# Kernel optimization log

Hardware: AMD Instinct MI355X
Metric: run time of the kernel (lower is better)

The kernel has to match this reference:

```python
import jax, jax.numpy as jnp
import numpy as np

# GemNet-OC hyperparameters (match init_kwargs)
CUTOFF = 6.0
NR = 128     # num_radial
NS = 7       # num_spherical
NB = 2       # num_blocks
DA = 256     # emb_size_atom
DE = 512     # emb_size_edge
DT = 64      # emb_size_trip
DC = 16      # emb_size_cbf/rbf
NRES_M = 2   # edge residual layers per block (before+after skip)
NRES_H = 2   # atom residual layers per block (num_atom)
N_ELEM = 119
INV_SQRT2 = 0.7071067811865476
_GAMMA = 0.5 / (CUTOFF / NR) ** 2  # gaussian rbf width


def _radial_basis(d):
    """Gaussian RBF with polynomial envelope (exponent 5). d: [E] -> [E, NR]."""
    u = d / CUTOFF
    p = 5.0
    env = 1.0 - (p + 1) * (p + 2) / 2 * u**5 + p * (p + 2) * u**6 - p * (p + 1) / 2 * u**7
    env = jnp.where(u < 1.0, env, 0.0)
    mu = jnp.linspace(0.0, CUTOFF, NR, dtype=d.dtype)
    return env[:, None] * jnp.exp(-_GAMMA * (d[:, None] - mu) ** 2)


def setup_inputs() -> dict:
    key = jax.random.key(0)
    ks = jax.random.split(key, 32)
    N, E, T = 8000, 100000, 500000

    atomic_numbers = jax.random.randint(ks[0], (N,), 0, N_ELEM)
    edge_index = jax.random.randint(ks[1], (2, E), 0, N)
    distances = jax.random.uniform(ks[2], (E,), jnp.float32, 0.5, CUTOFF)
    id3_ba = jax.random.randint(ks[3], (T,), 0, E)
    id3_ca = jax.random.randint(ks[4], (T,), 0, E)
    cos_angles = jax.random.uniform(ks[5], (T,), jnp.float32, -0.99, 0.99)

    def w(k, shape, fan_in):
        return jax.random.normal(k, shape, jnp.float32) / np.sqrt(fan_in)

    params = dict(
        atom_table=w(ks[6], (N_ELEM, DA), 1.0),
        W_edge=w(ks[7], (2 * DA + NR, DE), 2 * DA + NR), b_edge=jnp.zeros((DE,), jnp.float32),
        W_rbf3=w(ks[8], (NR, DC), NR),
        W_sph=w(ks[9], (NS, DC), NS),
        W_cbf_up=w(ks[10], (DC, DT), DC),
        W_rbf_h=w(ks[11], (NR, DE), NR),
        W_ba=w(ks[12], (NB, DE, DE), DE), b_ba=jnp.zeros((NB, DE), jnp.float32),
        W_down=w(ks[13], (NB, DE, DT), DE),
        W_trip_up=w(ks[14], (NB, DT, DE), DT),
        W_res_m=w(ks[15], (NB, NRES_M, 2, DE, DE), DE), b_res_m=jnp.zeros((NB, NRES_M, 2, DE), jnp.float32),
        W_e2a=w(ks[16], (NB, DE, DA), DE),
        W_res_h=w(ks[17], (NB, NRES_H, 2, DA, DA), DA), b_res_h=jnp.zeros((NB, NRES_H, 2, DA), jnp.float32),
        W_out=w(ks[18], (DA, 1), DA),
    )
    return dict(atomic_numbers=atomic_numbers, edge_index=edge_index, distances=distances,
                id3_ba=id3_ba, id3_ca=id3_ca, cos_angles=cos_angles, **params)


def reference(atomic_numbers, edge_index, distances, id3_ba, id3_ca, cos_angles,
              atom_table, W_edge, b_edge, W_rbf3, W_sph, W_cbf_up, W_rbf_h,
              W_ba, b_ba, W_down, W_trip_up, W_res_m, b_res_m, W_e2a,
              W_res_h, b_res_h, W_out):
    N = atomic_numbers.shape[0]
    E = distances.shape[0]
    silu = jax.nn.silu

    # --- shared basis functions ---
    rbf = _radial_basis(distances)                               # [E, NR]
    theta = jnp.arccos(jnp.clip(cos_angles, -1.0, 1.0))
    sph = jnp.cos(theta[:, None] * jnp.arange(NS, dtype=theta.dtype))  # [T, NS]
    # circular basis embedding: radial part (gathered per triplet) x angular part
    cbf_emb = (rbf @ W_rbf3)[id3_ba] * (sph @ W_sph)             # [T, DC]
    cbf_up = cbf_emb @ W_cbf_up                                  # [T, DT]
    rbf_h = rbf @ W_rbf_h                                        # [E, DE]

    # --- embeddings ---
    src, tgt = edge_index[0], edge_index[1]
    h = atom_table[atomic_numbers]                               # [N, DA]
    m = silu(jnp.concatenate([h[src], h[tgt], rbf], axis=-1) @ W_edge + b_edge)  # [E, DE]

    def residual(x, Wr, br):  # Wr: [2, D, D], br: [2, D]
        y = silu(x @ Wr[0] + br[0])
        y = silu(y @ Wr[1] + br[1])
        return (x + y) * INV_SQRT2

    # --- interaction blocks ---
    for b in range(NB):
        # triplet message passing (edge -> triplet gather, triplet -> edge scatter)
        x_ba = silu(m @ W_ba[b] + b_ba[b]) @ W_down[b]           # [E, DT]
        x3 = jax.ops.segment_sum(x_ba[id3_ba] * cbf_up, id3_ca, num_segments=E)  # [E, DT]
        m = (m + x3 @ W_trip_up[b]) * INV_SQRT2
        for r in range(NRES_M):
            m = residual(m, W_res_m[b, r], b_res_m[b, r])
        # atom update: rbf-scaled edge messages scattered onto target atoms
        h_msg = jax.ops.segment_sum((m * rbf_h) @ W_e2a[b], tgt, num_segments=N)  # [N, DA]
        h = h + h_msg
        for r in range(NRES_H):
            h = residual(h, W_res_h[b, r], b_res_h[b, r])

    # --- extensive energy output ---
    energy = jnp.sum(h @ W_out)
    return energy
```

## Files before the change

### kernel.cpp

```cpp
#include <hip/hip_runtime.h>
#include <hip/hip_bf16.h>
#include <math.h>

#define CUTOFF 6.0f
#define NRAD 128
#define NSPH 7
#define DA 256
#define DE 512
#define DT 64
#define DCB 16
#define INV_SQRT2 0.7071067811865476f
#define RBF_GAMMA 227.55555555555554f

typedef __hip_bfloat16 bf16;
typedef __bf16 bf16v;
typedef bf16v bf16x8 __attribute__((ext_vector_type(8)));
typedef float f32x4 __attribute__((ext_vector_type(4)));

static inline int cdiv(int a, int b) { return (a + b - 1) / b; }

__device__ __forceinline__ float silu_f(float v) {
    return v / (1.0f + __expf(-v));
}

__device__ __forceinline__ float to_f(float v) { return v; }
__device__ __forceinline__ float to_f(bf16 v) { return __bfloat162float(v); }

template<typename T> __device__ __forceinline__ T from_f(float v);
template<> __device__ __forceinline__ float from_f<float>(float v) { return v; }
template<> __device__ __forceinline__ bf16 from_f<bf16>(float v) { return __float2bfloat16(v); }

#if defined(__has_builtin)
#if __has_builtin(__builtin_amdgcn_global_load_lds)
#define HAS_GLD 1
#endif
#endif

#ifdef HAS_GLD
__device__ __forceinline__ void gld16(const bf16* g, bf16* l) {
    __builtin_amdgcn_global_load_lds(
        (const __attribute__((address_space(1))) void*)g,
        (__attribute__((address_space(3))) void*)l, 16, 0, 0);
}
#endif

template<typename TC, typename TD, int GMODE, bool PRE_ADD, bool HAS_BIAS,
         bool ACT, bool POST_ADD, bool POST_MUL>
__global__ __launch_bounds__(512, 8)
void gemm_mfma(const bf16* __restrict__ A, const bf16* __restrict__ A3,
               const bf16* __restrict__ Bt,
               TC* __restrict__ C, const TC* __restrict__ Cin,
               const TD* __restrict__ Dop, const float* __restrict__ bias,
               const int* __restrict__ idx1, const int* __restrict__ idx2,
               int M, int N, int K, int lda, int ldb, float scale)
{
    __shared__ bf16 As[128 * 32];
    __shared__ bf16 Bs[128 * 32];
    const int tid = threadIdx.x;

    const int nwg = gridDim.x * gridDim.y;
    const int bid = blockIdx.y * gridDim.x + blockIdx.x;
    const int q = nwg >> 3, r = nwg & 7;
    const int xcd = bid & 7, jj = bid >> 3;
    const int wg = (xcd < r) ? (xcd * (q + 1) + jj) : (r + xcd * q + jj);
    const int bn = (wg % gridDim.x) * 128;
    const int bm = (wg / gridDim.x) * 128;

    const int w   = tid >> 6;
    const int l   = tid & 63;
    const int l16 = l & 15;
    const int lr4 = (l >> 4) * 4;
    const int wr  = (w >> 2) * 64;
    const int wc  = (w & 3) * 32;
    const int koff = (((l >> 4) ^ ((l16 >> 1) & 3)) << 3);

    f32x4 acc[4][2];
#pragma unroll
    for (int i = 0; i < 4; ++i)
#pragma unroll
        for (int j = 0; j < 2; ++j) acc[i][j] = (f32x4){0.f, 0.f, 0.f, 0.f};

    const int csw = (((l & 3) ^ ((l >> 3) & 3)) << 3);
    const int rA = w * 16 + (l >> 2);

    int ar = bm + rA; if (ar >= M) ar = M - 1;
    const bf16* pAa = A + (long)((GMODE >= 2) ? idx1[ar] : ar) * lda + csw;
    const bf16* pAb = (GMODE >= 2) ? (A + (long)idx2[ar] * lda + csw) : pAa;
    const bf16* pAc = (GMODE == 3) ? (A3 + (long)ar * NRAD + csw) : pAa;

    int bc = bn + rA; if (bc >= N) bc = N - 1;
    const bf16* pB = Bt + (long)bc * ldb + csw;

    bf16* ldsA = As + (w * 16) * 32;
    bf16* ldsB = Bs + (w * 16) * 32;

    for (int k0 = 0; k0 < K; k0 += 32) {
        const bf16* a0;
        if (GMODE == 0) {
            a0 = pAa + k0;
        } else if (GMODE == 2) {
            a0 = (k0 >= DA) ? (pAb + (k0 - DA)) : (pAa + k0);
        } else {
            if (k0 >= 2 * DA)  a0 = pAc + (k0 - 2 * DA);
            else if (k0 >= DA) a0 = pAb + (k0 - DA);
            else               a0 = pAa + k0;
        }
#ifdef HAS_GLD
        gld16(a0, ldsA);
        gld16(pB + k0, ldsB);
#else
        *(uint4*)(ldsA + (l >> 2) * 32 + (l & 3) * 8) = *(const uint4*)a0;
        *(uint4*)(ldsB + (l >> 2) * 32 + (l & 3) * 8) = *(const uint4*)(pB + k0);
#endif
        __syncthreads();

        bf16x8 bfr[2];
#pragma unroll
        for (int fn = 0; fn < 2; ++fn)
            bfr[fn] = *(const bf16x8*)&Bs[(wc + fn * 16 + l16) * 32 + koff];
#pragma unroll
        for (int fm = 0; fm < 4; ++fm) {
            bf16x8 af = *(const bf16x8*)&As[(wr + fm * 16 + l16) * 32 + koff];
            acc[fm][0] = __builtin_amdgcn_mfma_f32_16x16x32_bf16(af, bfr[0], acc[fm][0], 0, 0, 0);
            acc[fm][1] = __builtin_amdgcn_mfma_f32_16x16x32_bf16(af, bfr[1], acc[fm][1], 0, 0, 0);
        }
        __syncthreads();
    }

#pragma unroll
    for (int fm = 0; fm < 4; ++fm) {
#pragma unroll
        for (int fn = 0; fn < 2; ++fn) {
            const int col = bn + wc + fn * 16 + l16;
            if (col < N) {
#pragma unroll
                for (int r4 = 0; r4 < 4; ++r4) {
                    const int row = bm + wr + fm * 16 + lr4 + r4;
                    if (row < M) {
                        float v = acc[fm][fn][r4];
                        if (PRE_ADD)  v += to_f(Cin[(long)row * N + col]);
                        if (HAS_BIAS) v += bias[col];
                        if (ACT)      v = silu_f(v);
                        if (POST_ADD) v += to_f(Dop[(long)row * N + col]);
                        if (POST_MUL) v *= to_f(Dop[(long)row * N + col]);
                        C[(long)row * N + col] = from_f<TC>(v * scale);
                    }
                }
            }
        }
    }
}

__global__ void f2b_kernel(const float* __restrict__ in, bf16* __restrict__ out, long n)
{
    long i = ((long)blockIdx.x * 256 + threadIdx.x) * 4;
    const long stride = (long)gridDim.x * 256 * 4;
    for (; i < n; i += stride) {
        float4 v = *(const float4*)(in + i);
        bf16 o[4] = {__float2bfloat16(v.x), __float2bfloat16(v.y),
                     __float2bfloat16(v.z), __float2bfloat16(v.w)};
        *(ushort4*)(out + i) = *(const ushort4*)o;
    }
}

__global__ __launch_bounds__(256)
void t2bT_kernel(const float* __restrict__ in, bf16* __restrict__ out, int K, int Nc)
{
    __shared__ float tile[32][33];
    const long bofs = (long)blockIdx.z * K * Nc;
    const int k0 = blockIdx.y * 32;
    const int n0 = blockIdx.x * 32;
    const int tx = threadIdx.x & 31;
    const int ty = threadIdx.x >> 5;
#pragma unroll
    for (int i = 0; i < 4; ++i) {
        int k = k0 + ty + 8 * i;
        tile[ty + 8 * i][tx] = (k < K && n0 + tx < Nc) ? in[bofs + (long)k * Nc + n0 + tx] : 0.f;
    }
    __syncthreads();
#pragma unroll
    for (int i = 0; i < 4; ++i) {
        int n = n0 + ty + 8 * i;
        if (n < Nc && k0 + tx < K)
            out[bofs + (long)n * K + k0 + tx] = from_f<bf16>(tile[tx][ty + 8 * i]);
    }
}

__global__ __launch_bounds__(128)
void basis_kernel(const float* __restrict__ dist,
                  const float* __restrict__ W_rbf3,
                  bf16* __restrict__ rbf, bf16* __restrict__ rbf3, int E)
{
    __shared__ float s_rbf[NRAD];
    const int e = blockIdx.x;
    if (e >= E) return;
    const int k = threadIdx.x;
    const float d = dist[e];
    const float u = d * (1.0f / CUTOFF);
    float u2 = u * u, u4 = u2 * u2, u5 = u4 * u, u6 = u5 * u, u7 = u6 * u;
    float env = 1.0f - 21.0f * u5 + 35.0f * u6 - 15.0f * u7;
    if (u >= 1.0f) env = 0.0f;
    const float mu = CUTOFF * (float)k / (float)(NRAD - 1);
    const float t = d - mu;
    const float v = env * __expf(-RBF_GAMMA * t * t);
    s_rbf[k] = v;
    rbf[(long)e * NRAD + k] = __float2bfloat16(v);
    __syncthreads();

    if (k < DCB) {
        float acc = 0.f;
        for (int kk = 0; kk < NRAD; ++kk) acc += s_rbf[kk] * W_rbf3[kk * DCB + k];
        rbf3[(long)e * DCB + k] = __float2bfloat16(acc);
    }
}

__global__ void h_init_kernel(const int* __restrict__ an,
                              const float* __restrict__ table,
                              float* __restrict__ h, int N)
{
    int i = blockIdx.x * 256 + threadIdx.x;
    if (i < N * DA) {
        int a = i >> 8;
        int c = i & 255;
        h[i] = table[(long)an[a] * DA + c];
    }
}

__global__ void zeroi_kernel(int* __restrict__ p, int n)
{
    int i = blockIdx.x * 256 + threadIdx.x;
    if (i < n) p[i] = 0;
}
__global__ void copyi_kernel(const int* __restrict__ a, int* __restrict__ b, int n)
{
    int i = blockIdx.x * 256 + threadIdx.x;
    if (i < n) b[i] = a[i];
}
__global__ void count_kernel(const int* __restrict__ idx, int* __restrict__ cnt, int n)
{
    int i = blockIdx.x * 256 + threadIdx.x;
    if (i < n) atomicAdd(&cnt[idx[i]], 1);
}
__global__ __launch_bounds__(256)
void seg_p1(const int* __restrict__ cnt, int* __restrict__ bsum, int n)
{
    __shared__ int s[256];
    int i = blockIdx.x * 256 + threadIdx.x;
    s[threadIdx.x] = (i < n) ? cnt[i] : 0;
    __syncthreads();
    for (int o = 128; o > 0; o >>= 1) {
        if (threadIdx.x < o) s[threadIdx.x] += s[threadIdx.x + o];
        __syncthreads();
    }
    if (threadIdx.x == 0) bsum[blockIdx.x] = s[0];
}
__global__ __launch_bounds__(1024)
void seg_p2(int* __restrict__ bsum, int* __restrict__ off, int nb, int n)
{
    __shared__ int s[1024];
    int v = (threadIdx.x < nb) ? bsum[threadIdx.x] : 0;
    s[threadIdx.x] = v;
    __syncthreads();
    for (int o = 1; o < 1024; o <<= 1) {
        int t = (threadIdx.x >= o) ? s[threadIdx.x - o] : 0;
        __syncthreads();
        s[threadIdx.x] += t;
        __syncthreads();
    }
    if (threadIdx.x < nb) bsum[threadIdx.x] = s[threadIdx.x] - v;
    if (threadIdx.x == nb - 1) off[n] = s[threadIdx.x];
}
__global__ __launch_bounds__(256)
void seg_p3(const int* __restrict__ cnt, const int* __restrict__ bsum,
            int* __restrict__ off, int n)
{
    __shared__ int s[256];
    int i = blockIdx.x * 256 + threadIdx.x;
    int v = (i < n) ? cnt[i] : 0;
    s[threadIdx.x] = v;
    __syncthreads();
    for (int o = 1; o < 256; o <<= 1) {
        int t = (threadIdx.x >= o) ? s[threadIdx.x - o] : 0;
        __syncthreads();
        s[threadIdx.x] += t;
        __syncthreads();
    }
    if (i < n) off[i] = bsum[blockIdx.x] + s[threadIdx.x] - v;
}
__global__ void fill_kernel(const int* __restrict__ idx, int* __restrict__ cur,
                            int* __restrict__ list, int n)
{
    int i = blockIdx.x * 256 + threadIdx.x;
    if (i < n) {
        int p = atomicAdd(&cur[idx[i]], 1);
        list[p] = i;
    }
}

__global__ __launch_bounds__(256)
void emb16_kernel(const float* __restrict__ cosang,
                  const int* __restrict__ id3_ba,
                  const bf16* __restrict__ rbf3,
                  const float* __restrict__ W_sph,
                  bf16* __restrict__ emb, int T)
{
    __shared__ float s_W[NSPH * DCB];
    const int tid = threadIdx.x;
    if (tid < NSPH * DCB) s_W[tid] = W_sph[tid];
    __syncthreads();
    const long idx = (long)blockIdx.x * 256 + tid;
    if (idx >= (long)T * DCB) return;
    const int t = (int)(idx >> 4);
    const int cc = (int)(idx & 15);
    float c = cosang[t];
    c = fminf(1.0f, fmaxf(-1.0f, c));
    float s0 = 1.0f, s1 = c;
    float a = s_W[0 * DCB + cc] + c * s_W[1 * DCB + cc];
#pragma unroll
    for (int s = 2; s < NSPH; ++s) {
        float s2 = 2.0f * c * s1 - s0;
        a += s2 * s_W[s * DCB + cc];
        s0 = s1; s1 = s2;
    }
    emb[idx] = __float2bfloat16(a * to_f(rbf3[(long)id3_ba[t] * DCB + cc]));
}

__global__ __launch_bounds__(256)
void x3_gather_kernel(const int* __restrict__ ca_off, const int* __restrict__ ca_list,
                      const int* __restrict__ id3_ba,
                      const bf16* __restrict__ emb, const bf16* __restrict__ xba,
                      const float* __restrict__ W_up,
                      bf16* __restrict__ x3, int E)
{
    __shared__ float s_Wup[DCB * DT];
    const int tid = threadIdx.x;
    for (int i = tid; i < DCB * DT; i += 256) s_Wup[i] = W_up[i];
    __syncthreads();
    const int e = blockIdx.x * 4 + (tid >> 6);
    const int d = tid & 63;
    if (e >= E) return;
    const int j0 = ca_off[e], j1 = ca_off[e + 1];
    float acc = 0.f;
    for (int j = j0; j < j1; ++j) {
        const int t = ca_list[j];
        const int ba = id3_ba[t];
        const ushort* ep = (const ushort*)(emb + (long)t * DCB);
        float dotv = 0.f;
#pragma unroll
        for (int cc = 0; cc < DCB; ++cc)
            dotv += __uint_as_float((unsigned)ep[cc] << 16) * s_Wup[cc * DT + d];
        acc += dotv * to_f(xba[(long)ba * DT + d]);
    }
    x3[(long)e * DT + d] = from_f<bf16>(acc);
}

__global__ __launch_bounds__(256)
void atom_segsum_kernel(const int* __restrict__ tgt_off, const int* __restrict__ tgt_list,
                        const bf16* __restrict__ g, bf16* __restrict__ s_out, int N)
{
    const int a = blockIdx.x;
    if (a >= N) return;
    const int c = threadIdx.x;
    float acc0 = 0.f, acc1 = 0.f;
    const int j0 = tgt_off[a], j1 = tgt_off[a + 1];
    for (int j = j0; j < j1; ++j) {
        const bf16* row = g + (long)tgt_list[j] * DE;
        acc0 += to_f(row[c]);
        acc1 += to_f(row[c + 256]);
    }
    s_out[(long)a * DE + c]       = from_f<bf16>(acc0);
    s_out[(long)a * DE + c + 256] = from_f<bf16>(acc1);
}

__global__ __launch_bounds__(256)
void reduce1_kernel(const float* __restrict__ h, const float* __restrict__ Wout,
                    float* __restrict__ partials, int N)
{
    __shared__ float s[256];
    const int a0 = blockIdx.x * 32;
    const int col = threadIdx.x;
    float acc = 0.f;
    for (int a = 0; a < 32; ++a) {
        int row = a0 + a;
        if (row < N) acc += h[(long)row * DA + col];
    }
    acc *= Wout[col];
    s[col] = acc;
    __syncthreads();
    for (int off = 128; off > 0; off >>= 1) {
        if (col < off) s[col] += s[col + off];
        __syncthreads();
    }
    if (col == 0) partials[blockIdx.x] = s[0];
}

__global__ __launch_bounds__(256)
void reduce2_kernel(const float* __restrict__ partials, float* __restrict__ out, int nb)
{
    __shared__ float s[256];
    float acc = 0.f;
    for (int i = threadIdx.x; i < nb; i += 256) acc += partials[i];
    s[threadIdx.x] = acc;
    __syncthreads();
    for (int off = 128; off > 0; off >>= 1) {
        if (threadIdx.x < off) s[threadIdx.x] += s[threadIdx.x + off];
        __syncthreads();
    }
    if (threadIdx.x == 0) out[0] = s[0];
}

__global__ void diag_kernel(float* out, float v) { out[0] = v; }

extern "C" void kernel_launch(void* const* d_in, const int* in_sizes, int n_in,
                              void* d_out, int out_size, void* d_ws, size_t ws_size,
                              hipStream_t stream)
{
    const int*   atomic_numbers = (const int*)d_in[0];
    const int*   edge_index     = (const int*)d_in[1];
    const float* distances      = (const float*)d_in[2];
    const int*   id3_ba         = (const int*)d_in[3];
    const int*   id3_ca         = (const int*)d_in[4];
    const float* cos_angles     = (const float*)d_in[5];
    const float* atom_table     = (const float*)d_in[6];
    const float* W_edge         = (const float*)d_in[7];
    const float* b_edge         = (const float*)d_in[8];
    const float* W_rbf3         = (const float*)d_in[9];
    const float* W_sph          = (const float*)d_in[10];
    const float* W_cbf_up       = (const float*)d_in[11];
    const float* W_rbf_h        = (const float*)d_in[12];
    const float* W_ba           = (const float*)d_in[13];
    const float* b_ba           = (const float*)d_in[14];
    const float* W_down         = (const float*)d_in[15];
    const float* W_trip_up      = (const float*)d_in[16];
    const float* W_res_m        = (const float*)d_in[17];
    const float* b_res_m        = (const float*)d_in[18];
    const float* W_e2a          = (const float*)d_in[19];
    const float* W_res_h        = (const float*)d_in[20];
    const float* b_res_h        = (const float*)d_in[21];
    const float* W_out          = (const float*)d_in[22];

    const int N = in_sizes[0];
    const int E = in_sizes[2];
    const int T = in_sizes[3];
    const int* src = edge_index;
    const int* tgt = edge_index + E;

    char* base = (char*)d_ws;
    size_t off = 0;
    auto alloc = [&](size_t bytes) -> void* {
        void* r = base + off;
        off += (bytes + 255) & ~(size_t)255;
        return r;
    };
    bf16*  m     = (bf16*)alloc((size_t)E * DE * 2);
    bf16*  t1    = (bf16*)alloc((size_t)E * DE * 2);
    bf16*  rbf   = (bf16*)alloc((size_t)E * NRAD * 2);
    bf16*  rbf3  = (bf16*)alloc((size_t)E * DCB * 2);
    bf16*  xba   = (bf16*)alloc((size_t)E * DT * 2);
    float* h     = (float*)alloc((size_t)N * DA * 4);
    float* partials = (float*)alloc(4096 * 4);
    bf16* wedgeT = (bf16*)alloc((size_t)DE * (2 * DA + NRAD) * 2);
    bf16* wbaT   = (bf16*)alloc((size_t)2 * DE * DE * 2);
    bf16* wdownT = (bf16*)alloc((size_t)2 * DT * DE * 2);
    bf16* wtripT = (bf16*)alloc((size_t)2 * DE * DT * 2);
    bf16* wresmT = (bf16*)alloc((size_t)8 * DE * DE * 2);
    bf16* we2aT  = (bf16*)alloc((size_t)2 * DA * DE * 2);
    bf16* wrbfhT = (bf16*)alloc((size_t)DE * NRAD * 2);
    bf16* h_bf   = (bf16*)alloc((size_t)N * DA * 2);
    int* tgt_off  = (int*)alloc((size_t)(N + 1) * 4);
    int* tgt_list = (int*)alloc((size_t)E * 4);
    int* ca_off   = (int*)alloc((size_t)(E + 1) * 4);
    int* ca_list  = (int*)alloc((size_t)T * 4);
    bf16*  x3b    = t1;
    bf16*  emb16  = (bf16*)((char*)t1 + 20000000);
    bf16*  wreshT = (bf16*)((char*)t1 + 40000000);
    int*   cur_a  = (int*)t1;
    int*   cur_b  = (int*)((char*)t1 + 4000000);
    int*   bsum   = (int*)((char*)t1 + 8000000);
    bf16*  s_bf   = xba;
    bf16*  tmph_b = xba;

    if (off > ws_size) {
        diag_kernel<<<1, 1, 0, stream>>>((float*)d_out, (float)(ws_size >> 20));
        return;
    }

    const dim3 blk(256);
    const dim3 blk5(512);

    { dim3 g(DE / 32, (2 * DA + NRAD) / 32, 1);
      t2bT_kernel<<<g, blk, 0, stream>>>(W_edge, wedgeT, 2 * DA + NRAD, DE); }
    { dim3 g(DE / 32, DE / 32, 2);
      t2bT_kernel<<<g, blk, 0, stream>>>(W_ba, wbaT, DE, DE); }
    { dim3 g(DT / 32, DE / 32, 2);
      t2bT_kernel<<<g, blk, 0, stream>>>(W_down, wdownT, DE, DT); }
    { dim3 g(DE / 32, DT / 32, 2);
      t2bT_kernel<<<g, blk, 0, stream>>>(W_trip_up, wtripT, DT, DE); }
    { dim3 g(DE / 32, DE / 32, 8);
      t2bT_kernel<<<g, blk, 0, stream>>>(W_res_m, wresmT, DE, DE); }
    { dim3 g(DA / 32, DE / 32, 2);
      t2bT_kernel<<<g, blk, 0, stream>>>(W_e2a, we2aT, DE, DA); }
    { dim3 g(DE / 32, NRAD / 32, 1);
      t2bT_kernel<<<g, blk, 0, stream>>>(W_rbf_h, wrbfhT, NRAD, DE); }

    {
        zeroi_kernel<<<cdiv(N, 256), blk, 0, stream>>>(cur_a, N);
        count_kernel<<<cdiv(E, 256), blk, 0, stream>>>(tgt, cur_a, E);
        seg_p1<<<cdiv(N, 256), blk, 0, stream>>>(cur_a, bsum, N);
        seg_p2<<<1, 1024, 0, stream>>>(bsum, tgt_off, cdiv(N, 256), N);
        seg_p3<<<cdiv(N, 256), blk, 0, stream>>>(cur_a, bsum, tgt_off, N);
        copyi_kernel<<<cdiv(N, 256), blk, 0, stream>>>(tgt_off, cur_a, N);
        fill_kernel<<<cdiv(E, 256), blk, 0, stream>>>(tgt, cur_a, tgt_list, E);
        zeroi_kernel<<<cdiv(E, 256), blk, 0, stream>>>(cur_b, E);
        count_kernel<<<cdiv(T, 256), blk, 0, stream>>>(id3_ca, cur_b, T);
        seg_p1<<<cdiv(E, 256), blk, 0, stream>>>(cur_b, bsum, E);
        seg_p2<<<1, 1024, 0, stream>>>(bsum, ca_off, cdiv(E, 256), E);
        seg_p3<<<cdiv(E, 256), blk, 0, stream>>>(cur_b, bsum, ca_off, E);
        copyi_kernel<<<cdiv(E, 256), blk, 0, stream>>>(ca_off, cur_b, E);
        fill_kernel<<<cdiv(T, 256), blk, 0, stream>>>(id3_ca, cur_b, ca_list, T);
    }

    basis_kernel<<<E, 128, 0, stream>>>(distances, W_rbf3, rbf, rbf3, E);
    h_init_kernel<<<cdiv(N * DA, 256), blk, 0, stream>>>(atomic_numbers, atom_table, h, N);
    f2b_kernel<<<256, blk, 0, stream>>>(h, h_bf, (long)N * DA);

    {
        dim3 g(cdiv(DE, 128), cdiv(E, 128));
        gemm_mfma<bf16, bf16, 3, false, true, true, false, false>
            <<<g, blk5, 0, stream>>>(h_bf, rbf, wedgeT, m, nullptr, nullptr, b_edge,
                                     src, tgt, E, DE, 2 * DA + NRAD, DA, 2 * DA + NRAD, 1.0f);
    }

    for (int b = 0; b < 2; ++b) {
        const bf16* WbaT = wbaT + (long)b * DE * DE;
        const float* bba = b_ba + (long)b * DE;
        const bf16* WdnT = wdownT + (long)b * DT * DE;
        const bf16* WtuT = wtripT + (long)b * DE * DT;
        const bf16* We2aT = we2aT + (long)b * DA * DE;

        {
            dim3 g(cdiv(DE, 128), cdiv(E, 128));
            gemm_mfma<bf16, bf16, 0, false, true, true, false, false>
                <<<g, blk5, 0, stream>>>(m, nullptr, WbaT, t1, nullptr, (const bf16*)nullptr,
                                         bba, nullptr, nullptr, E, DE, DE, DE, DE, 1.0f);
        }
        {
            dim3 g(cdiv(DT, 128), cdiv(E, 128));
            gemm_mfma<bf16, bf16, 0, false, false, false, false, false>
                <<<g, blk5, 0, stream>>>(t1, nullptr, WdnT, xba, nullptr, (const bf16*)nullptr,
                                         nullptr, nullptr, nullptr, E, DT, DE, DE, DE, 1.0f);
        }
        emb16_kernel<<<cdiv(T * DCB, 256), blk, 0, stream>>>(cos_angles, id3_ba, rbf3,
                                                             W_sph, emb16, T);
        x3_gather_kernel<<<cdiv(E, 4), blk, 0, stream>>>(ca_off, ca_list, id3_ba,
                                                         emb16, xba, W_cbf_up, x3b, E);
        {
            dim3 g(cdiv(DE, 128), cdiv(E, 128));
            gemm_mfma<bf16, bf16, 0, true, false, false, false, false>
                <<<g, blk5, 0, stream>>>(x3b, nullptr, WtuT, m, m, (const bf16*)nullptr,
                                         nullptr, nullptr, nullptr, E, DE, DT, DT, DT, INV_SQRT2);
        }
        for (int r = 0; r < 2; ++r) {
            const bf16* W0T = wresmT + (((long)b * 2 + r) * 2 + 0) * DE * DE;
            const bf16* W1T = wresmT + (((long)b * 2 + r) * 2 + 1) * DE * DE;
            const float* b0 = b_res_m + (((long)b * 2 + r) * 2 + 0) * DE;
            const float* b1 = b_res_m + (((long)b * 2 + r) * 2 + 1) * DE;
            dim3 g(cdiv(DE, 128), cdiv(E, 128));
            gemm_mfma<bf16, bf16, 0, false, true, true, false, false>
                <<<g, blk5, 0, stream>>>(m, nullptr, W0T, t1, nullptr, (const bf16*)nullptr,
                                         b0, nullptr, nullptr, E, DE, DE, DE, DE, 1.0f);
            gemm_mfma<bf16, bf16, 0, false, true, true, true, false>
                <<<g, blk5, 0, stream>>>(t1, nullptr, W1T, m, nullptr, m, b1,
                                         nullptr, nullptr, E, DE, DE, DE, DE, INV_SQRT2);
        }
        {
            dim3 g(cdiv(DE, 128), cdiv(E, 128));
            gemm_mfma<bf16, bf16, 0, false, false, false, false, true>
                <<<g, blk5, 0, stream>>>(rbf, nullptr, wrbfhT, t1, nullptr, m, nullptr,
                                         nullptr, nullptr, E, DE, NRAD, NRAD, NRAD, 1.0f);
        }
        atom_segsum_kernel<<<N, blk, 0, stream>>>(tgt_off, tgt_list, t1, s_bf, N);
        {
            dim3 g(cdiv(DA, 128), cdiv(N, 128));
            gemm_mfma<float, float, 0, true, false, false, false, false>
                <<<g, blk5, 0, stream>>>(s_bf, nullptr, We2aT, h, h, (const float*)nullptr,
                                         nullptr, nullptr, nullptr, N, DA, DE, DE, DE, 1.0f);
        }
        {
            dim3 gt(DA / 32, DA / 32, 4);
            t2bT_kernel<<<gt, blk, 0, stream>>>(W_res_h + (long)b * 4 * DA * DA,
                                                wreshT, DA, DA);
        }
        for (int r = 0; r < 2; ++r) {
            const bf16* W0T = wreshT + (long)(r * 2 + 0) * DA * DA;
            const bf16* W1T = wreshT + (long)(r * 2 + 1) * DA * DA;
            const float* b0 = b_res_h + (((long)b * 2 + r) * 2 + 0) * DA;
            const float* b1 = b_res_h + (((long)b * 2 + r) * 2 + 1) * DA;
            f2b_kernel<<<256, blk, 0, stream>>>(h, h_bf, (long)N * DA);
            dim3 g(cdiv(DA, 128), cdiv(N, 128));
            gemm_mfma<bf16, bf16, 0, false, true, true, false, false>
                <<<g, blk5, 0, stream>>>(h_bf, nullptr, W0T, tmph_b, nullptr,
                                         (const bf16*)nullptr, b0, nullptr, nullptr,
                                         N, DA, DA, DA, DA, 1.0f);
            gemm_mfma<float, float, 0, false, true, true, true, false>
                <<<g, blk5, 0, stream>>>(tmph_b, nullptr, W1T, h, nullptr, h, b1,
                                         nullptr, nullptr, N, DA, DA, DA, DA, INV_SQRT2);
        }
    }

    const int nb1 = cdiv(N, 32);
    reduce1_kernel<<<nb1, blk, 0, stream>>>(h, W_out, partials, N);
    reduce2_kernel<<<1, blk, 0, stream>>>(partials, (float*)d_out, nb1);
}
```

Before: 2.083 ms.

## Triple-buffer LDS tiles with async global_load_lds prefetch in GEMM

Replaces the single-buffered A/B shared-memory tiles with a three-stage ring buffer. Tiles are prefetched two K-steps ahead via global_load_lds, and explicit vmcnt waits plus s_barrier replace the two __syncthreads per iteration, so global loads overlap the MFMA compute. This uses three times the LDS (48 KB per workgroup) and lowers the launch-bounds occupancy hint from 8 to 6, trading occupancy for latency hiding. The fallback path now indexes staging by tid instead of the lane and wave offset.

```diff
diff --git a/kernel.cpp b/kernel.cpp
--- a/kernel.cpp
+++ b/kernel.cpp
@@ -46,7 +46,7 @@
 
 template<typename TC, typename TD, int GMODE, bool PRE_ADD, bool HAS_BIAS,
          bool ACT, bool POST_ADD, bool POST_MUL>
-__global__ __launch_bounds__(512, 8)
+__global__ __launch_bounds__(512, 6)
 void gemm_mfma(const bf16* __restrict__ A, const bf16* __restrict__ A3,
                const bf16* __restrict__ Bt,
                TC* __restrict__ C, const TC* __restrict__ Cin,
@@ -54,8 +54,7 @@
                const int* __restrict__ idx1, const int* __restrict__ idx2,
                int M, int N, int K, int lda, int ldb, float scale)
 {
-    __shared__ bf16 As[128 * 32];
-    __shared__ bf16 Bs[128 * 32];
+    __shared__ bf16 lds[3 * 8192];
     const int tid = threadIdx.x;
 
     const int nwg = gridDim.x * gridDim.y;
@@ -91,10 +90,9 @@
     int bc = bn + rA; if (bc >= N) bc = N - 1;
     const bf16* pB = Bt + (long)bc * ldb + csw;
 
-    bf16* ldsA = As + (w * 16) * 32;
-    bf16* ldsB = Bs + (w * 16) * 32;
-
-    for (int k0 = 0; k0 < K; k0 += 32) {
+    const int wofs = (w * 16) * 32;
+
+    auto STAGE = [&](int k0, int bo) {
         const bf16* a0;
         if (GMODE == 0) {
             a0 = pAa + k0;
@@ -106,26 +104,59 @@
             else               a0 = pAa + k0;
         }
 #ifdef HAS_GLD
-        gld16(a0, ldsA);
-        gld16(pB + k0, ldsB);
+        gld16(a0, lds + bo + wofs);
+        gld16(pB + k0, lds + bo + 4096 + wofs);
 #else
-        *(uint4*)(ldsA + (l >> 2) * 32 + (l & 3) * 8) = *(const uint4*)a0;
-        *(uint4*)(ldsB + (l >> 2) * 32 + (l & 3) * 8) = *(const uint4*)(pB + k0);
+        *(uint4*)(lds + bo + (tid >> 2) * 32 + (tid & 3) * 8) = *(const uint4*)a0;
+        *(uint4*)(lds + bo + 4096 + (tid >> 2) * 32 + (tid & 3) * 8) = *(const uint4*)(pB + k0);
 #endif
-        __syncthreads();
-
+    };
+
+    auto COMPUTE = [&](int bo) {
+        const bf16* As_ = lds + bo;
+        const bf16* Bs_ = lds + bo + 4096;
         bf16x8 bfr[2];
 #pragma unroll
         for (int fn = 0; fn < 2; ++fn)
-            bfr[fn] = *(const bf16x8*)&Bs[(wc + fn * 16 + l16) * 32 + koff];
+            bfr[fn] = *(const bf16x8*)&Bs_[(wc + fn * 16 + l16) * 32 + koff];
 #pragma unroll
         for (int fm = 0; fm < 4; ++fm) {
-            bf16x8 af = *(const bf16x8*)&As[(wr + fm * 16 + l16) * 32 + koff];
+            bf16x8 af = *(const bf16x8*)&As_[(wr + fm * 16 + l16) * 32 + koff];
             acc[fm][0] = __builtin_amdgcn_mfma_f32_16x16x32_bf16(af, bfr[0], acc[fm][0], 0, 0, 0);
             acc[fm][1] = __builtin_amdgcn_mfma_f32_16x16x32_bf16(af, bfr[1], acc[fm][1], 0, 0, 0);
         }
-        __syncthreads();
-    }
+    };
+
+    const int nt = K >> 5;
+
+#ifdef HAS_GLD
+    if (nt > 0) STAGE(0, 0);
+    if (nt > 1) STAGE(32, 8192);
+    int boC = 0;
+    int boS = 16384;
+    for (int t = 0; t < nt; ++t) {
+        if (t + 2 < nt) STAGE((t + 2) << 5, boS);
+        const int rem = nt - 1 - t;
+        __builtin_amdgcn_sched_barrier(0);
+        if (rem >= 2)      asm volatile("s_waitcnt vmcnt(4)" ::: "memory");
+        else if (rem == 1) asm volatile("s_waitcnt vmcnt(2)" ::: "memory");
+        else               asm volatile("s_waitcnt vmcnt(0)" ::: "memory");
+        __builtin_amdgcn_sched_barrier(0);
+        __builtin_amdgcn_s_barrier();
+        __builtin_amdgcn_sched_barrier(0);
+        COMPUTE(boC);
+        __builtin_amdgcn_s_barrier();
+        boC += 8192; if (boC > 16384) boC = 0;
+        boS += 8192; if (boS > 16384) boS = 0;
+    }
+#else
+    for (int t = 0; t < nt; ++t) {
+        STAGE(t << 5, 0);
+        __syncthreads();
+        COMPUTE(0);
+        __syncthreads();
+    }
+#endif
 
 #pragma unroll
     for (int fm = 0; fm < 4; ++fm) {
```

Result: no change. 2.075 ms, median of 3 (-0.4%).
